# Optimization experiments

Measured on AMD Instinct MI355X. Metric: run time of the kernel, lower is better.

The kernel has to match this reference:

```python
import jax, jax.numpy as jnp
import numpy as np

IN_CH, OUT_CH = 384, 512


def setup_inputs() -> dict:
    key = jax.random.key(0)
    ks = jax.random.split(key, 9)
    B, C, H, W = 8, IN_CH, 48, 48
    s_in = 1.0 / np.sqrt(IN_CH)
    s_out = 1.0 / np.sqrt(OUT_CH)
    return {
        "x": jax.random.normal(ks[0], (B, C, H, W), dtype=jnp.float32),
        "Wq": jax.random.uniform(ks[1], (OUT_CH, IN_CH), jnp.float32, -s_in, s_in),
        "bq": jax.random.uniform(ks[2], (OUT_CH,), jnp.float32, -s_in, s_in),
        "Wk": jax.random.uniform(ks[3], (OUT_CH, IN_CH), jnp.float32, -s_in, s_in),
        "bk": jax.random.uniform(ks[4], (OUT_CH,), jnp.float32, -s_in, s_in),
        "Wv": jax.random.uniform(ks[5], (OUT_CH, IN_CH), jnp.float32, -s_in, s_in),
        "bv": jax.random.uniform(ks[6], (OUT_CH,), jnp.float32, -s_in, s_in),
        "Wo": jax.random.uniform(ks[7], (OUT_CH, OUT_CH), jnp.float32, -s_out, s_out),
        "bo": jax.random.uniform(ks[8], (OUT_CH,), jnp.float32, -s_out, s_out),
    }


def reference(x, Wq, bq, Wk, bk, Wv, bv, Wo, bo):
    B, C, H, W = x.shape
    N = H * W  # number of spatial tokens
    xf = x.reshape(B, C, N)  # [B, C, N]
    # 1x1 convs == per-pixel linear projections
    q = jnp.einsum('oc,bcn->bno', Wq, xf) + bq  # [B, N, O]
    k = jnp.einsum('oc,bcn->bon', Wk, xf) + bk[None, :, None]  # [B, O, N]
    v = jnp.einsum('oc,bcn->bon', Wv, xf) + bv[None, :, None]  # [B, O, N]
    scale = 1.0 / jnp.sqrt(jnp.asarray(Wq.shape[0], x.dtype))
    attn = jax.nn.softmax(jnp.einsum('bno,bom->bnm', q, k) * scale, axis=-1)  # [B, N, N]
    out = jnp.einsum('bom,bnm->bon', v, attn)  # [B, O, N]
    out = jnp.einsum('po,bon->bpn', Wo, out) + bo[None, :, None]
    return out.reshape(B, Wo.shape[0], H, W)
```

## Files before the change

### kernel.cpp

```cpp
#include <hip/hip_runtime.h>
#include <hip/hip_bf16.h>
#include <stdint.h>

#define B_    8
#define CIN   384
#define OCH   512
#define NTOK  2304
#define SCALE 0.044194173824159216f

typedef unsigned short u16;
typedef u16   u16x8 __attribute__((ext_vector_type(8)));
typedef u16   u16x4 __attribute__((ext_vector_type(4)));
typedef short s16x8 __attribute__((ext_vector_type(8)));
typedef float f32x4 __attribute__((ext_vector_type(4)));

__device__ __forceinline__ float bf2f(u16 u) {
    union { uint32_t i; float f; } v; v.i = ((uint32_t)u) << 16; return v.f;
}
__device__ __forceinline__ u16 f2bf(float f) {
    union { uint32_t i; float f; } v; v.f = f;
    uint32_t r = v.i + 0x7fffu + ((v.i >> 16) & 1u);
    return (u16)(r >> 16);
}

typedef __attribute__((address_space(1))) const uint32_t glb_u32;
typedef __attribute__((address_space(3))) uint32_t lds_u32;

__device__ __forceinline__ void stage_async(const u16* __restrict__ src, int ld,
                                            u16* __restrict__ dst, int t)
{
    const int lane = t & 63;
    const int w = t >> 6;
#pragma unroll
    for (int it = 0; it < 2; ++it) {
        const int chunk = w * 2 + it;
        const int r = chunk * 16 + (lane >> 2);
        const int c = (lane & 3) * 8;
        const u16* gp = src + (size_t)r * ld + c;
        u16* lp = dst + chunk * 512;
        __builtin_amdgcn_global_load_lds((glb_u32*)gp, (lds_u32*)lp, 16, 0, 0);
    }
}

__device__ __forceinline__ void mfma_core(const u16 (* __restrict__ As)[32],
                                          const u16 (* __restrict__ Bs)[32],
                                          int wm, int wn, int lrow, int kq,
                                          f32x4 acc[4][4])
{
    s16x8 a[4], b[4];
#pragma unroll
    for (int i = 0; i < 4; ++i)
        a[i] = *(const s16x8*)&As[wm + i * 16 + lrow][kq * 8];
#pragma unroll
    for (int j = 0; j < 4; ++j)
        b[j] = *(const s16x8*)&Bs[wn + j * 16 + lrow][kq * 8];
#pragma unroll
    for (int i = 0; i < 4; ++i)
#pragma unroll
        for (int j = 0; j < 4; ++j)
            acc[i][j] = __builtin_amdgcn_mfma_f32_16x16x32_bf16(a[i], b[j], acc[i][j], 0, 0, 0);
}

#define WQKV_SZ (OCH * CIN)
#define WO_SZ   (OCH * OCH)
#define WTOT    (3 * WQKV_SZ + WO_SZ)

__global__ __launch_bounds__(256) void prep_w_kernel(
    const float* __restrict__ Wq, const float* __restrict__ Wk,
    const float* __restrict__ Wv, const float* __restrict__ Wo,
    u16* __restrict__ Wqb, u16* __restrict__ Wkb,
    u16* __restrict__ Wvb, u16* __restrict__ Wob)
{
    const int i4 = (blockIdx.x * 256 + threadIdx.x) * 4;
    if (i4 >= WTOT) return;
    const float* src; u16* dst; int off;
    if      (i4 < WQKV_SZ)     { src = Wq; dst = Wqb; off = i4; }
    else if (i4 < 2 * WQKV_SZ) { src = Wk; dst = Wkb; off = i4 - WQKV_SZ; }
    else if (i4 < 3 * WQKV_SZ) { src = Wv; dst = Wvb; off = i4 - 2 * WQKV_SZ; }
    else                       { src = Wo; dst = Wob; off = i4 - 3 * WQKV_SZ; }
    float4 v = *(const float4*)(src + off);
    u16x4 o;
    o.x = f2bf(v.x); o.y = f2bf(v.y); o.z = f2bf(v.z); o.w = f2bf(v.w);
    *(u16x4*)(dst + off) = o;
}

__global__ __launch_bounds__(256) void transpose_x_kernel(
    const float* __restrict__ x, u16* __restrict__ xT)
{
    const int n0 = blockIdx.x * 64;
    const int c0 = blockIdx.y * 64;
    const int b  = blockIdx.z;
    const float* X = x + (size_t)b * CIN * NTOK;

    __shared__ float Ts[64][66];

    const int t = threadIdx.x;
#pragma unroll
    for (int rep = 0; rep < 4; ++rep) {
        const int cr = (t >> 4) + rep * 16;
        const int n4 = (t & 15) * 4;
        float4 v = *(const float4*)(X + (size_t)(c0 + cr) * NTOK + n0 + n4);
        *(float2*)&Ts[cr][n4]     = make_float2(v.x, v.y);
        *(float2*)&Ts[cr][n4 + 2] = make_float2(v.z, v.w);
    }
    __syncthreads();

    u16* O = xT + (size_t)b * NTOK * CIN;
#pragma unroll
    for (int rep = 0; rep < 2; ++rep) {
        const int nr = (t >> 3) + rep * 32;
        const int c8 = (t & 7) * 8;
        u16 tmp[8];
#pragma unroll
        for (int j = 0; j < 8; ++j) tmp[j] = f2bf(Ts[c8 + j][nr]);
        *(u16x8*)(O + (size_t)(n0 + nr) * CIN + c0 + c8) = *(const u16x8*)tmp;
    }
}

template <int BIAS, typename OutT>
__global__ __launch_bounds__(256) void gemm_kernel(
    const u16* __restrict__ Ag, const u16* __restrict__ Bg,
    const float* __restrict__ bias, OutT* __restrict__ Cg,
    int K, int N, long sA, long sB, long sC)
{
    const int n0 = blockIdx.x * 128;
    const int m0 = blockIdx.y * 128;
    const int z  = blockIdx.z;
    const u16* A  = Ag + (size_t)z * sA + (size_t)m0 * K;
    const u16* Bp = Bg + (size_t)z * sB + (size_t)n0 * K;
    OutT* C = Cg + (size_t)z * sC;

    __shared__ u16 As[128][32];
    __shared__ u16 Bs[128][32];

    const int t = threadIdx.x;
    const int w = t >> 6, ln = t & 63;
    const int wm = (w & 1) * 64, wn = (w >> 1) * 64;
    const int lrow = ln & 15, kq = ln >> 4;

    f32x4 acc[4][4] = {};

    for (int k0 = 0; k0 < K; k0 += 32) {
        stage_async(A + k0, K, &As[0][0], t);
        stage_async(Bp + k0, K, &Bs[0][0], t);
        __syncthreads();
        mfma_core(As, Bs, wm, wn, lrow, kq, acc);
        __syncthreads();
    }

#pragma unroll
    for (int i = 0; i < 4; ++i) {
        const int row = m0 + wm + i * 16 + kq * 4;
#pragma unroll
        for (int r = 0; r < 4; ++r) {
            float badd = 0.f;
            if (BIAS == 1) badd = bias[row + r];
#pragma unroll
            for (int j = 0; j < 4; ++j) {
                const int col = n0 + wn + j * 16 + lrow;
                float v = acc[i][j][r];
                if (BIAS == 1) v += badd;
                if (BIAS == 2) v += bias[col];
                if constexpr (sizeof(OutT) == 2)
                    C[(size_t)(row + r) * N + col] = f2bf(v);
                else
                    C[(size_t)(row + r) * N + col] = v;
            }
        }
    }
}

__global__ __launch_bounds__(256) void logits_exp_kernel(
    const u16* __restrict__ Qt, const u16* __restrict__ Kt,
    u16* __restrict__ Ew, float* __restrict__ rowsumG)
{
    const int n0 = blockIdx.x * 128;
    const int m0 = blockIdx.y * 128;
    const int z  = blockIdx.z;
    const u16* A  = Qt + (size_t)z * NTOK * OCH + (size_t)m0 * OCH;
    const u16* Bp = Kt + (size_t)z * NTOK * OCH + (size_t)n0 * OCH;

    __shared__ u16 As[128][32];
    __shared__ u16 Bs[128][32];
    __shared__ float rowsumL[128];

    const int t = threadIdx.x;
    const int w = t >> 6, ln = t & 63;
    const int wm = (w & 1) * 64, wn = (w >> 1) * 64;
    const int lrow = ln & 15, kq = ln >> 4;

    if (t < 128) rowsumL[t] = 0.f;

    f32x4 acc[4][4] = {};

    for (int k0 = 0; k0 < OCH; k0 += 32) {
        stage_async(A + k0, OCH, &As[0][0], t);
        stage_async(Bp + k0, OCH, &Bs[0][0], t);
        __syncthreads();
        mfma_core(As, Bs, wm, wn, lrow, kq, acc);
        __syncthreads();
    }

    u16* E = Ew + (size_t)z * NTOK * NTOK;
#pragma unroll
    for (int i = 0; i < 4; ++i) {
        const int row = m0 + wm + i * 16 + kq * 4;
#pragma unroll
        for (int r = 0; r < 4; ++r) {
            float part = 0.f;
#pragma unroll
            for (int j = 0; j < 4; ++j) {
                const int col = n0 + wn + j * 16 + lrow;
                float e = __expf(acc[i][j][r] * SCALE);
                part += e;
                E[(size_t)(row + r) * NTOK + col] = f2bf(e);
            }
            part += __shfl_xor(part, 1);
            part += __shfl_xor(part, 2);
            part += __shfl_xor(part, 4);
            part += __shfl_xor(part, 8);
            if (lrow == 0) atomicAdd(&rowsumL[wm + i * 16 + kq * 4 + r], part);
        }
    }
    __syncthreads();
    if (t < 128) atomicAdd(&rowsumG[(size_t)z * NTOK + m0 + t], rowsumL[t]);
}

__global__ __launch_bounds__(256) void pv_div_kernel(
    const u16* __restrict__ Ew, const u16* __restrict__ Vw,
    const float* __restrict__ rowsumG, u16* __restrict__ AOt)
{
    const int n0 = blockIdx.x * 128;
    const int m0 = blockIdx.y * 128;
    const int z  = blockIdx.z;
    const u16* A  = Ew + (size_t)z * NTOK * NTOK + (size_t)m0 * NTOK;
    const u16* Bp = Vw + (size_t)z * OCH * NTOK + (size_t)n0 * NTOK;

    __shared__ u16 As[128][32];
    __shared__ u16 Bs[128][32];

    const int t = threadIdx.x;
    const int w = t >> 6, ln = t & 63;
    const int wm = (w & 1) * 64, wn = (w >> 1) * 64;
    const int lrow = ln & 15, kq = ln >> 4;

    f32x4 acc[4][4] = {};

    for (int k0 = 0; k0 < NTOK; k0 += 32) {
        stage_async(A + k0, NTOK, &As[0][0], t);
        stage_async(Bp + k0, NTOK, &Bs[0][0], t);
        __syncthreads();
        mfma_core(As, Bs, wm, wn, lrow, kq, acc);
        __syncthreads();
    }

    u16* AO = AOt + (size_t)z * NTOK * OCH;
#pragma unroll
    for (int i = 0; i < 4; ++i) {
        const int row = m0 + wm + i * 16 + kq * 4;
#pragma unroll
        for (int r = 0; r < 4; ++r) {
            const float inv = 1.0f / rowsumG[(size_t)z * NTOK + row + r];
#pragma unroll
            for (int j = 0; j < 4; ++j) {
                const int col = n0 + wn + j * 16 + lrow;
                AO[(size_t)(row + r) * OCH + col] = f2bf(acc[i][j][r] * inv);
            }
        }
    }
}

extern "C" void kernel_launch(void* const* d_in, const int* in_sizes, int n_in,
                              void* d_out, int out_size, void* d_ws, size_t ws_size,
                              hipStream_t stream)
{
    const float* x  = (const float*)d_in[0];
    const float* Wq = (const float*)d_in[1];
    const float* bq = (const float*)d_in[2];
    const float* Wk = (const float*)d_in[3];
    const float* bk = (const float*)d_in[4];
    const float* Wv = (const float*)d_in[5];
    const float* bv = (const float*)d_in[6];
    const float* Wo = (const float*)d_in[7];
    const float* bo = (const float*)d_in[8];
    float* out = (float*)d_out;

    u16* ws = (u16*)d_ws;
    u16* Wqb = ws;
    u16* Wkb = Wqb + WQKV_SZ;
    u16* Wvb = Wkb + WQKV_SZ;
    u16* Wob = Wvb + WQKV_SZ;
    u16* xT  = Wob + WO_SZ;
    const size_t xtsz  = (size_t)B_ * NTOK * CIN;
    const size_t qkvsz = (size_t)B_ * NTOK * OCH;
    u16* Qt  = xT + xtsz;
    u16* Kt  = Qt + qkvsz;
    u16* Vw  = Kt + qkvsz;
    u16* Ew  = Vw + qkvsz;
    float* rowsumG = (float*)(Ew + (size_t)B_ * NTOK * NTOK);
    u16* AOt = Qt;

    dim3 blk(256);

    prep_w_kernel<<<dim3((WTOT / 4 + 255) / 256), blk, 0, stream>>>(
        Wq, Wk, Wv, Wo, Wqb, Wkb, Wvb, Wob);
    transpose_x_kernel<<<dim3(NTOK / 64, CIN / 64, B_), blk, 0, stream>>>(x, xT);
    hipMemsetAsync(rowsumG, 0, (size_t)B_ * NTOK * sizeof(float), stream);

    gemm_kernel<2, u16><<<dim3(OCH / 128, NTOK / 128, B_), blk, 0, stream>>>(
        xT, Wqb, bq, Qt, CIN, OCH, (long)NTOK * CIN, 0L, (long)NTOK * OCH);
    gemm_kernel<2, u16><<<dim3(OCH / 128, NTOK / 128, B_), blk, 0, stream>>>(
        xT, Wkb, bk, Kt, CIN, OCH, (long)NTOK * CIN, 0L, (long)NTOK * OCH);
    gemm_kernel<1, u16><<<dim3(NTOK / 128, OCH / 128, B_), blk, 0, stream>>>(
        Wvb, xT, bv, Vw, CIN, NTOK, 0L, (long)NTOK * CIN, (long)OCH * NTOK);

    logits_exp_kernel<<<dim3(NTOK / 128, NTOK / 128, B_), blk, 0, stream>>>(
        Qt, Kt, Ew, rowsumG);

    pv_div_kernel<<<dim3(OCH / 128, NTOK / 128, B_), blk, 0, stream>>>(
        Ew, Vw, rowsumG, AOt);

    gemm_kernel<1, float><<<dim3(NTOK / 128, OCH / 128, B_), blk, 0, stream>>>(
        Wob, AOt, bo, out, OCH, NTOK, 0L, (long)NTOK * OCH, (long)OCH * NTOK);
}
```

Before: 323.4 us.

## Double K-tile to 64 with MFMA-fragment LDS layout and batch-interleaved 1D grid

All GEMM-style kernels now stage a 128x64 K-slab per iteration instead of 128x32. Data is stored in LDS in a fragment-major order so each lane's 16-byte MFMA operand is contiguous, which halves the number of barriers per K and is meant to reduce LDS bank conflicts. The launch grid is flattened to 1D with the batch index varying fastest, so blocks that run at the same time share the same weight and tile rows in L2. LDS use per block doubles to 32 KB, which could lower occupancy.

```diff
diff --git a/kernel.cpp b/kernel.cpp
--- a/kernel.cpp
+++ b/kernel.cpp
@@ -26,39 +26,44 @@
 typedef __attribute__((address_space(1))) const uint32_t glb_u32;
 typedef __attribute__((address_space(3))) uint32_t lds_u32;
 
-__device__ __forceinline__ void stage_async(const u16* __restrict__ src, int ld,
-                                            u16* __restrict__ dst, int t)
+__device__ __forceinline__ void stage_async64(const u16* __restrict__ src, int ld,
+                                              u16* __restrict__ dst, int t)
 {
     const int lane = t & 63;
     const int w = t >> 6;
-#pragma unroll
-    for (int it = 0; it < 2; ++it) {
-        const int chunk = w * 2 + it;
-        const int r = chunk * 16 + (lane >> 2);
-        const int c = (lane & 3) * 8;
-        const u16* gp = src + (size_t)r * ld + c;
-        u16* lp = dst + chunk * 512;
+    const int kq = lane >> 4;
+    const int lrow = lane & 15;
+#pragma unroll
+    for (int it = 0; it < 4; ++it) {
+        const int ck  = w * 4 + it;
+        const int row = (ck & 7) * 16 + lrow;
+        const int col = ((ck >> 3) * 4 + kq) * 8;
+        const u16* gp = src + (size_t)row * ld + col;
+        u16* lp = dst + ck * 512;
         __builtin_amdgcn_global_load_lds((glb_u32*)gp, (lds_u32*)lp, 16, 0, 0);
     }
 }
 
-__device__ __forceinline__ void mfma_core(const u16 (* __restrict__ As)[32],
-                                          const u16 (* __restrict__ Bs)[32],
-                                          int wm, int wn, int lrow, int kq,
-                                          f32x4 acc[4][4])
-{
-    s16x8 a[4], b[4];
-#pragma unroll
-    for (int i = 0; i < 4; ++i)
-        a[i] = *(const s16x8*)&As[wm + i * 16 + lrow][kq * 8];
-#pragma unroll
-    for (int j = 0; j < 4; ++j)
-        b[j] = *(const s16x8*)&Bs[wn + j * 16 + lrow][kq * 8];
-#pragma unroll
-    for (int i = 0; i < 4; ++i)
+__device__ __forceinline__ void mfma_core64(const u16* __restrict__ As,
+                                            const u16* __restrict__ Bs,
+                                            int wm, int wn, int lrow, int kq,
+                                            f32x4 acc[4][4])
+{
+#pragma unroll
+    for (int h = 0; h < 2; ++h) {
+        s16x8 a[4], b[4];
+#pragma unroll
+        for (int i = 0; i < 4; ++i)
+            a[i] = *(const s16x8*)(As + (((h * 8 + (wm >> 4) + i) * 64) + kq * 16 + lrow) * 8);
 #pragma unroll
         for (int j = 0; j < 4; ++j)
-            acc[i][j] = __builtin_amdgcn_mfma_f32_16x16x32_bf16(a[i], b[j], acc[i][j], 0, 0, 0);
+            b[j] = *(const s16x8*)(Bs + (((h * 8 + (wn >> 4) + j) * 64) + kq * 16 + lrow) * 8);
+#pragma unroll
+        for (int i = 0; i < 4; ++i)
+#pragma unroll
+            for (int j = 0; j < 4; ++j)
+                acc[i][j] = __builtin_amdgcn_mfma_f32_16x16x32_bf16(a[i], b[j], acc[i][j], 0, 0, 0);
+    }
 }
 
 #define WQKV_SZ (OCH * CIN)
@@ -121,17 +126,18 @@
 __global__ __launch_bounds__(256) void gemm_kernel(
     const u16* __restrict__ Ag, const u16* __restrict__ Bg,
     const float* __restrict__ bias, OutT* __restrict__ Cg,
-    int K, int N, long sA, long sB, long sC)
-{
-    const int n0 = blockIdx.x * 128;
-    const int m0 = blockIdx.y * 128;
-    const int z  = blockIdx.z;
+    int K, int N, long sA, long sB, long sC, int GX, int GZ)
+{
+    const int z   = blockIdx.x % GZ;
+    const int rem = blockIdx.x / GZ;
+    const int n0 = (rem % GX) * 128;
+    const int m0 = (rem / GX) * 128;
     const u16* A  = Ag + (size_t)z * sA + (size_t)m0 * K;
     const u16* Bp = Bg + (size_t)z * sB + (size_t)n0 * K;
     OutT* C = Cg + (size_t)z * sC;
 
-    __shared__ u16 As[128][32];
-    __shared__ u16 Bs[128][32];
+    __shared__ u16 As[128 * 64];
+    __shared__ u16 Bs[128 * 64];
 
     const int t = threadIdx.x;
     const int w = t >> 6, ln = t & 63;
@@ -140,11 +146,11 @@
 
     f32x4 acc[4][4] = {};
 
-    for (int k0 = 0; k0 < K; k0 += 32) {
-        stage_async(A + k0, K, &As[0][0], t);
-        stage_async(Bp + k0, K, &Bs[0][0], t);
-        __syncthreads();
-        mfma_core(As, Bs, wm, wn, lrow, kq, acc);
+    for (int k0 = 0; k0 < K; k0 += 64) {
+        stage_async64(A + k0, K, As, t);
+        stage_async64(Bp + k0, K, Bs, t);
+        __syncthreads();
+        mfma_core64(As, Bs, wm, wn, lrow, kq, acc);
         __syncthreads();
     }
 
@@ -174,14 +180,15 @@
     const u16* __restrict__ Qt, const u16* __restrict__ Kt,
     u16* __restrict__ Ew, float* __restrict__ rowsumG)
 {
-    const int n0 = blockIdx.x * 128;
-    const int m0 = blockIdx.y * 128;
-    const int z  = blockIdx.z;
+    const int z   = blockIdx.x % B_;
+    const int rem = blockIdx.x / B_;
+    const int n0 = (rem % (NTOK / 128)) * 128;
+    const int m0 = (rem / (NTOK / 128)) * 128;
     const u16* A  = Qt + (size_t)z * NTOK * OCH + (size_t)m0 * OCH;
     const u16* Bp = Kt + (size_t)z * NTOK * OCH + (size_t)n0 * OCH;
 
-    __shared__ u16 As[128][32];
-    __shared__ u16 Bs[128][32];
+    __shared__ u16 As[128 * 64];
+    __shared__ u16 Bs[128 * 64];
     __shared__ float rowsumL[128];
 
     const int t = threadIdx.x;
@@ -193,11 +200,11 @@
 
     f32x4 acc[4][4] = {};
 
-    for (int k0 = 0; k0 < OCH; k0 += 32) {
-        stage_async(A + k0, OCH, &As[0][0], t);
-        stage_async(Bp + k0, OCH, &Bs[0][0], t);
-        __syncthreads();
-        mfma_core(As, Bs, wm, wn, lrow, kq, acc);
+    for (int k0 = 0; k0 < OCH; k0 += 64) {
+        stage_async64(A + k0, OCH, As, t);
+        stage_async64(Bp + k0, OCH, Bs, t);
+        __syncthreads();
+        mfma_core64(As, Bs, wm, wn, lrow, kq, acc);
         __syncthreads();
     }
 
@@ -230,14 +237,15 @@
     const u16* __restrict__ Ew, const u16* __restrict__ Vw,
     const float* __restrict__ rowsumG, u16* __restrict__ AOt)
 {
-    const int n0 = blockIdx.x * 128;
-    const int m0 = blockIdx.y * 128;
-    const int z  = blockIdx.z;
+    const int z   = blockIdx.x % B_;
+    const int rem = blockIdx.x / B_;
+    const int n0 = (rem % (OCH / 128)) * 128;
+    const int m0 = (rem / (OCH / 128)) * 128;
     const u16* A  = Ew + (size_t)z * NTOK * NTOK + (size_t)m0 * NTOK;
     const u16* Bp = Vw + (size_t)z * OCH * NTOK + (size_t)n0 * NTOK;
 
-    __shared__ u16 As[128][32];
-    __shared__ u16 Bs[128][32];
+    __shared__ u16 As[128 * 64];
+    __shared__ u16 Bs[128 * 64];
 
     const int t = threadIdx.x;
     const int w = t >> 6, ln = t & 63;
@@ -246,11 +254,11 @@
 
     f32x4 acc[4][4] = {};
 
-    for (int k0 = 0; k0 < NTOK; k0 += 32) {
-        stage_async(A + k0, NTOK, &As[0][0], t);
-        stage_async(Bp + k0, NTOK, &Bs[0][0], t);
-        __syncthreads();
-        mfma_core(As, Bs, wm, wn, lrow, kq, acc);
+    for (int k0 = 0; k0 < NTOK; k0 += 64) {
+        stage_async64(A + k0, NTOK, As, t);
+        stage_async64(Bp + k0, NTOK, Bs, t);
+        __syncthreads();
+        mfma_core64(As, Bs, wm, wn, lrow, kq, acc);
         __syncthreads();
     }
 
@@ -307,19 +315,17 @@
     transpose_x_kernel<<<dim3(NTOK / 64, CIN / 64, B_), blk, 0, stream>>>(x, xT);
     hipMemsetAsync(rowsumG, 0, (size_t)B_ * NTOK * sizeof(float), stream);
 
-    gemm_kernel<2, u16><<<dim3(OCH / 128, NTOK / 128, B_), blk, 0, stream>>>(
-        xT, Wqb, bq, Qt, CIN, OCH, (long)NTOK * CIN, 0L, (long)NTOK * OCH);
-    gemm_kernel<2, u16><<<dim3(OCH / 128, NTOK / 128, B_), blk, 0, stream>>>(
-        xT, Wkb, bk, Kt, CIN, OCH, (long)NTOK * CIN, 0L, (long)NTOK * OCH);
-    gemm_kernel<1, u16><<<dim3(NTOK / 128, OCH / 128, B_), blk, 0, stream>>>(
-        Wvb, xT, bv, Vw, CIN, NTOK, 0L, (long)NTOK * CIN, (long)OCH * NTOK);
-
-    logits_exp_kernel<<<dim3(NTOK / 128, NTOK / 128, B_), blk, 0, stream>>>(
-        Qt, Kt, Ew, rowsumG);
-
-    pv_div_kernel<<<dim3(OCH / 128, NTOK / 128, B_), blk, 0, stream>>>(
-        Ew, Vw, rowsumG, AOt);
-
-    gemm_kernel<1, float><<<dim3(NTOK / 128, OCH / 128, B_), blk, 0, stream>>>(
-        Wob, AOt, bo, out, OCH, NTOK, 0L, (long)NTOK * OCH, (long)OCH * NTOK);
-}
+    gemm_kernel<2, u16><<<dim3(4 * 18 * B_), blk, 0, stream>>>(
+        xT, Wqb, bq, Qt, CIN, OCH, (long)NTOK * CIN, 0L, (long)NTOK * OCH, 4, B_);
+    gemm_kernel<2, u16><<<dim3(4 * 18 * B_), blk, 0, stream>>>(
+        xT, Wkb, bk, Kt, CIN, OCH, (long)NTOK * CIN, 0L, (long)NTOK * OCH, 4, B_);
+    gemm_kernel<1, u16><<<dim3(18 * 4 * B_), blk, 0, stream>>>(
+        Wvb, xT, bv, Vw, CIN, NTOK, 0L, (long)NTOK * CIN, (long)OCH * NTOK, 18, B_);
+
+    logits_exp_kernel<<<dim3(18 * 18 * B_), blk, 0, stream>>>(Qt, Kt, Ew, rowsumG);
+
+    pv_div_kernel<<<dim3(4 * 18 * B_), blk, 0, stream>>>(Ew, Vw, rowsumG, AOt);
+
+    gemm_kernel<1, float><<<dim3(18 * 4 * B_), blk, 0, stream>>>(
+        Wob, AOt, bo, out, OCH, NTOK, 0L, (long)NTOK * OCH, (long)OCH * NTOK, 18, B_);
+}
```

Result: slower. 446.5 us (+38.1%).
